# Optimization experiments

Hardware: AMD Instinct MI355X
Metric: run time of the kernel (lower is better)

## Reference

```python
import jax, jax.numpy as jnp
import numpy as np

LN_EPS = 1e-12


def setup_inputs() -> dict:
    key = jax.random.key(0)
    ks = jax.random.split(key, 10)
    B, S, W, D, H = 16, 512, 5, 200, 768
    std = 0.02
    return {
        "layer_output": jax.random.normal(ks[0], (B, S, H), dtype=jnp.float32),
        "word_embeddings": jax.random.normal(ks[1], (B, S, W, D), dtype=jnp.float32),
        "word_mask": jax.random.randint(ks[2], (B, S, W), 0, 2, dtype=jnp.int64),
        "W1": jax.random.normal(ks[3], (D, H), dtype=jnp.float32) * std,
        "b1": jnp.zeros((H,), dtype=jnp.float32),
        "W2": jax.random.normal(ks[4], (H, H), dtype=jnp.float32) * std,
        "b2": jnp.zeros((H,), dtype=jnp.float32),
        "attn_W": jax.random.normal(ks[5], (H, H), dtype=jnp.float32) * std,
        "ln_gamma": jnp.ones((H,), dtype=jnp.float32),
        "ln_beta": jnp.zeros((H,), dtype=jnp.float32),
    }


def reference(layer_output, word_embeddings, word_mask, W1, b1, W2, b2, attn_W, ln_gamma, ln_beta):
    # word_transform: Linear -> Tanh -> Linear (dropout = identity in eval)
    we = jnp.tanh(jnp.einsum("bswd,dh->bswh", word_embeddings, W1) + b1)
    we = jnp.einsum("bswh,hk->bswk", we, W2) + b2  # [B,S,W,H]

    # bilinear word attention: (x @ attn_W) . word_outputs -> score over W
    q = jnp.einsum("bsh,hk->bsk", layer_output, attn_W)  # [B,S,H]
    alpha = jnp.einsum("bsk,bswk->bsw", q, we)            # [B,S,W]
    alpha = alpha + (1.0 - word_mask.astype(alpha.dtype)) * -10000.0
    alpha = jax.nn.softmax(alpha, axis=-1)

    # weighted sum over words + residual
    agg = jnp.einsum("bsw,bswh->bsh", alpha, we)
    h = layer_output + agg

    # LayerNorm (fuse_layer; dropout = identity in eval)
    mu = jnp.mean(h, axis=-1, keepdims=True)
    var = jnp.mean(jnp.square(h - mu), axis=-1, keepdims=True)
    return (h - mu) * jax.lax.rsqrt(var + LN_EPS) * ln_gamma + ln_beta
```

## Files before the change

### kernel.cpp

```cpp
#include <hip/hip_runtime.h>
#include <hip/hip_bf16.h>
#include <math.h>


typedef __attribute__((ext_vector_type(8))) short bf16x8;
typedef __attribute__((ext_vector_type(4))) float f32x4;

__device__ __forceinline__ unsigned short f2bf_bits(float f) {
    __hip_bfloat16 h = __float2bfloat16(f);
    return *reinterpret_cast<unsigned short*>(&h);
}
__device__ __forceinline__ float bf_bits2f(unsigned short u) {
    union { unsigned int i; float f; } v; v.i = ((unsigned int)u) << 16; return v.f;
}
__device__ __forceinline__ float tanh_fast(float x) {
    float xc = fminf(fmaxf(x, -9.f), 9.f);
    float t  = __expf(2.f * xc);
    return (t - 1.f) * __builtin_amdgcn_rcpf(t + 1.f);
}

__device__ __forceinline__ void async_cp16(const void* g, void* lds) {
#if __has_builtin(__builtin_amdgcn_global_load_lds)
    auto gp = (const __attribute__((address_space(1))) unsigned int*)g;
    auto lp = (__attribute__((address_space(3))) unsigned int*)lds;
    __builtin_amdgcn_global_load_lds(gp, lp, 16, 0, 0);
#else
    *(uint4*)lds = *(const uint4*)g;
#endif
}

template<bool HAS_BIAS, bool TANH_ACT, bool RESID, bool OUT_BF16, int N, int K>
__global__ __launch_bounds__(256) void mfma_gemm(
    const __hip_bfloat16* __restrict__ A,
    const __hip_bfloat16* __restrict__ Bt,
    const float* __restrict__ bias,
    const float* __restrict__ resid,
    void* __restrict__ outp)
{
    __shared__ __align__(16) unsigned short As[128 * 32];
    __shared__ __align__(16) unsigned short Bs[128 * 32];
    const int tid  = threadIdx.x;
    const int lane = tid & 63;
    const int wave = tid >> 6;
    const int wm   = wave & 1;
    const int wn   = wave >> 1;
    const int m0   = blockIdx.y * 128;
    const int n0   = blockIdx.x * 128;

    const int srow  = lane >> 2;
    const int skoff = (lane & 3) * 8;
    const __hip_bfloat16* gA = A  + (size_t)(m0 + wave * 32 + srow) * K + skoff;
    const __hip_bfloat16* gB = Bt + (size_t)(n0 + wave * 32 + srow) * K + skoff;
    unsigned short* lA = &As[wave * 1024 + lane * 8];
    unsigned short* lB = &Bs[wave * 1024 + lane * 8];

    const int row16 = lane & 15;
    const int kq    = lane >> 4;

    f32x4 acc[4][4];
#pragma unroll
    for (int i = 0; i < 4; i++)
#pragma unroll
        for (int j = 0; j < 4; j++) acc[i][j] = (f32x4){0.f, 0.f, 0.f, 0.f};

    for (int k0 = 0; k0 < K; k0 += 32) {
        async_cp16(gA,          lA);
        async_cp16(gA + 16 * K, lA + 512);
        async_cp16(gB,          lB);
        async_cp16(gB + 16 * K, lB + 512);
        gA += 32; gB += 32;
        __syncthreads();

        bf16x8 af[4], bg[4];
#pragma unroll
        for (int mi = 0; mi < 4; mi++)
            af[mi] = *(const bf16x8*)&As[(wm * 64 + mi * 16 + row16) * 32 + kq * 8];
#pragma unroll
        for (int ni = 0; ni < 4; ni++)
            bg[ni] = *(const bf16x8*)&Bs[(wn * 64 + ni * 16 + row16) * 32 + kq * 8];
#pragma unroll
        for (int mi = 0; mi < 4; mi++)
#pragma unroll
            for (int ni = 0; ni < 4; ni++)
                acc[mi][ni] = __builtin_amdgcn_mfma_f32_16x16x32_bf16(
                    af[mi], bg[ni], acc[mi][ni], 0, 0, 0);
        __syncthreads();
    }

#pragma unroll
    for (int ni = 0; ni < 4; ni++) {
        const int gcol = n0 + wn * 64 + ni * 16 + row16;
        float bcol = 0.f;
        if (HAS_BIAS) bcol = bias[gcol];
#pragma unroll
        for (int mi = 0; mi < 4; mi++) {
#pragma unroll
            for (int r = 0; r < 4; r++) {
                const int grow = m0 + wm * 64 + mi * 16 + kq * 4 + r;
                float v = acc[mi][ni][r];
                if (HAS_BIAS) v += bcol;
                if (TANH_ACT) v = tanh_fast(v);
                if (RESID)    v += resid[(size_t)grow * N + gcol];
                if (OUT_BF16) ((__hip_bfloat16*)outp)[(size_t)grow * N + gcol] = __float2bfloat16(v);
                else          ((float*)outp)[(size_t)grow * N + gcol] = v;
            }
        }
    }
}

__global__ __launch_bounds__(256) void cvt_all(
    const float* __restrict__ x,  __hip_bfloat16* __restrict__ xb,
    const float* __restrict__ w2, __hip_bfloat16* __restrict__ w2b,
    const float* __restrict__ aw, __hip_bfloat16* __restrict__ awb)
{
    const int NX = 8192 * 768 / 4;
    const int NW = 768 * 768 / 4;
    long long i = (long long)blockIdx.x * 256 + threadIdx.x;
    const float* src; __hip_bfloat16* dst;
    if (i < NX)           { src = x;  dst = xb;  }
    else if (i < NX + NW) { src = w2; dst = w2b; i -= NX; }
    else                  { src = aw; dst = awb; i -= NX + NW; if (i >= NW) return; }
    float4 v = ((const float4*)src)[i];
    ((ushort4*)dst)[i] = make_ushort4(f2bf_bits(v.x), f2bf_bits(v.y), f2bf_bits(v.z), f2bf_bits(v.w));
}

__global__ __launch_bounds__(256) void cvt_padE(const float* __restrict__ E,
                                                __hip_bfloat16* __restrict__ Eb)
{
    const int row = blockIdx.x, k = threadIdx.x;
    if (k < 224) {
        float v = (k < 200) ? E[(size_t)row * 200 + k] : 0.f;
        Eb[(size_t)row * 224 + k] = __float2bfloat16(v);
    }
}

__global__ __launch_bounds__(256) void transpose_cvt(const float* __restrict__ in,
                                                     __hip_bfloat16* __restrict__ out,
                                                     int R, int C, int Rpad)
{
    __shared__ float tile[32][33];
    const int c0 = blockIdx.x * 32, r0 = blockIdx.y * 32;
    const int x = threadIdx.x, y = threadIdx.y;
#pragma unroll
    for (int i = 0; i < 32; i += 8) {
        int r = r0 + y + i;
        tile[y + i][x] = (r < R) ? in[(size_t)r * C + c0 + x] : 0.f;
    }
    __syncthreads();
#pragma unroll
    for (int i = 0; i < 32; i += 8)
        out[(size_t)(c0 + y + i) * Rpad + r0 + x] = __float2bfloat16(tile[x][y + i]);
}

__global__ __launch_bounds__(256) void attn_kernel(
    const __hip_bfloat16* __restrict__ T,
    const __hip_bfloat16* P,
    const int* __restrict__ mask,
    __hip_bfloat16* S)
{
    const int lane = threadIdx.x & 63;
    const int wave = threadIdx.x >> 6;
    const int r    = blockIdx.x * 4 + wave;
    const int base = lane * 12;

    float pv[12];
    {
        const ushort4* pp = (const ushort4*)((const unsigned short*)P + (size_t)r * 768 + base);
        ushort4 u0 = pp[0], u1 = pp[1], u2 = pp[2];
        unsigned short us[12] = {u0.x,u0.y,u0.z,u0.w, u1.x,u1.y,u1.z,u1.w, u2.x,u2.y,u2.z,u2.w};
#pragma unroll
        for (int j = 0; j < 12; j++) pv[j] = bf_bits2f(us[j]);
    }
    float tv[5][12], part[5];
#pragma unroll
    for (int w = 0; w < 5; w++) {
        const ushort4* tp = (const ushort4*)((const unsigned short*)T + ((size_t)r * 5 + w) * 768 + base);
        ushort4 u0 = tp[0], u1 = tp[1], u2 = tp[2];
        unsigned short us[12] = {u0.x,u0.y,u0.z,u0.w, u1.x,u1.y,u1.z,u1.w, u2.x,u2.y,u2.z,u2.w};
        float s = 0.f;
#pragma unroll
        for (int j = 0; j < 12; j++) { tv[w][j] = bf_bits2f(us[j]); s += tv[w][j] * pv[j]; }
        part[w] = s;
    }
#pragma unroll
    for (int off = 32; off > 0; off >>= 1)
#pragma unroll
        for (int w = 0; w < 5; w++)
            part[w] += __shfl_xor(part[w], off, 64);

    float logit[5], mx = -1e30f;
#pragma unroll
    for (int w = 0; w < 5; w++) {
        float m = (float)mask[(size_t)r * 5 + w];
        logit[w] = part[w] - 10000.0f * (1.0f - m);
        mx = fmaxf(mx, logit[w]);
    }
    float se = 0.f;
#pragma unroll
    for (int w = 0; w < 5; w++) { logit[w] = expf(logit[w] - mx); se += logit[w]; }
    const float inv = 1.0f / se;

    unsigned short os[12];
#pragma unroll
    for (int j = 0; j < 12; j++) {
        float s = 0.f;
#pragma unroll
        for (int w = 0; w < 5; w++) s += logit[w] * tv[w][j];
        os[j] = f2bf_bits(s * inv);
    }
    ushort4* sp = (ushort4*)((unsigned short*)S + (size_t)r * 768 + base);
    sp[0] = make_ushort4(os[0], os[1], os[2],  os[3]);
    sp[1] = make_ushort4(os[4], os[5], os[6],  os[7]);
    sp[2] = make_ushort4(os[8], os[9], os[10], os[11]);
}

__global__ __launch_bounds__(256) void ln_kernel(
    const float* __restrict__ Hbuf, const float* __restrict__ gamma,
    const float* __restrict__ beta, float* __restrict__ out)
{
    const int r = blockIdx.x, t = threadIdx.x;
    __shared__ float red[256];
    float v[3];
    float s = 0.f;
#pragma unroll
    for (int c = 0; c < 3; c++) { v[c] = Hbuf[(size_t)r * 768 + t + 256 * c]; s += v[c]; }
    red[t] = s; __syncthreads();
    for (int off = 128; off > 0; off >>= 1) { if (t < off) red[t] += red[t + off]; __syncthreads(); }
    const float mu = red[0] * (1.f / 768.f);
    __syncthreads();
    float vs = 0.f;
#pragma unroll
    for (int c = 0; c < 3; c++) { float d = v[c] - mu; vs += d * d; }
    red[t] = vs; __syncthreads();
    for (int off = 128; off > 0; off >>= 1) { if (t < off) red[t] += red[t + off]; __syncthreads(); }
    const float var = red[0] * (1.f / 768.f);
    const float rs = rsqrtf(var + 1e-12f);
#pragma unroll
    for (int c = 0; c < 3; c++) {
        int h = t + 256 * c;
        out[(size_t)r * 768 + h] = (v[c] - mu) * rs * gamma[h] + beta[h];
    }
}

extern "C" void kernel_launch(void* const* d_in, const int* in_sizes, int n_in,
                              void* d_out, int out_size, void* d_ws, size_t ws_size,
                              hipStream_t stream)
{
    const float* x      = (const float*)d_in[0];
    const float* E      = (const float*)d_in[1];
    const int*   mask   = (const int*)d_in[2];
    const float* W1     = (const float*)d_in[3];
    const float* b1     = (const float*)d_in[4];
    const float* W2     = (const float*)d_in[5];
    const float* b2     = (const float*)d_in[6];
    const float* attn_W = (const float*)d_in[7];
    const float* gamma  = (const float*)d_in[8];
    const float* beta   = (const float*)d_in[9];
    float* out = (float*)d_out;

    const int BS = 8192, H = 768, M1 = 40960, KP = 224;

    char* p = (char*)d_ws;
    auto alloc = [&](size_t bytes) { char* q = p; p += (bytes + 255) & ~(size_t)255; return q; };
    __hip_bfloat16* xb    = (__hip_bfloat16*)alloc((size_t)BS * H * 2);
    __hip_bfloat16* W2b   = (__hip_bfloat16*)alloc((size_t)H * H * 2);
    __hip_bfloat16* W2Tb  = (__hip_bfloat16*)alloc((size_t)H * H * 2);
    __hip_bfloat16* attnb = (__hip_bfloat16*)alloc((size_t)H * H * 2);
    __hip_bfloat16* Ctb   = (__hip_bfloat16*)alloc((size_t)H * H * 2);
    __hip_bfloat16* W1Tb  = (__hip_bfloat16*)alloc((size_t)H * KP * 2);
    __hip_bfloat16* Tb    = (__hip_bfloat16*)alloc((size_t)M1 * H * 2);
    __hip_bfloat16* Eb    = (__hip_bfloat16*)alloc((size_t)M1 * KP * 2);
    float* Hb = (float*)Tb;
    __hip_bfloat16* Pb = Eb;
    __hip_bfloat16* Sb = Pb;

    cvt_all<<<6144 + 576 + 576, 256, 0, stream>>>(x, xb, W2, W2b, attn_W, attnb);
    cvt_padE<<<M1, 256, 0, stream>>>(E, Eb);
    transpose_cvt<<<dim3(24, 7),  dim3(32, 8), 0, stream>>>(W1, W1Tb, 200, H, KP);
    transpose_cvt<<<dim3(24, 24), dim3(32, 8), 0, stream>>>(W2, W2Tb, H, H, H);

    mfma_gemm<false, false, false, true, 768, 768><<<dim3(6, 6), 256, 0, stream>>>(
        W2b, attnb, nullptr, nullptr, Ctb);
    mfma_gemm<true, true, false, true, 768, 224><<<dim3(6, 320), 256, 0, stream>>>(
        Eb, W1Tb, b1, nullptr, Tb);
    mfma_gemm<false, false, false, true, 768, 768><<<dim3(6, 64), 256, 0, stream>>>(
        xb, Ctb, nullptr, nullptr, Pb);
    attn_kernel<<<BS / 4, 256, 0, stream>>>(Tb, Pb, mask, Sb);
    mfma_gemm<true, false, true, false, 768, 768><<<dim3(6, 64), 256, 0, stream>>>(
        Sb, W2Tb, b2, x, Hb);
    ln_kernel<<<BS, 256, 0, stream>>>(Hb, gamma, beta, out);
}
```

Before: 264.5 us.

## Stage GEMM epilogue through LDS, remap blocks per XCD, vectorize LN and padding

The GEMM epilogue now writes results into shared memory and then stores coalesced 16-byte rows to global memory, with the residual loaded as float4. Blocks are launched on a 1D grid and remapped so consecutive tiles land on the same XCD for better L2 reuse. cvt_padE and ln_kernel are rewritten to process one row per wave with vectorized loads and wave shuffles instead of LDS tree reductions. The cost is extra LDS traffic and barriers in the epilogue, and a larger 32KB shared allocation that may reduce occupancy.

Measured after the change: 242.1 us. 1.09x faster.

```diff
diff --git a/kernel.cpp b/kernel.cpp
--- a/kernel.cpp
+++ b/kernel.cpp
@@ -29,7 +29,7 @@
 #endif
 }
 
-template<bool HAS_BIAS, bool TANH_ACT, bool RESID, bool OUT_BF16, int N, int K>
+template<bool HAS_BIAS, bool TANH_ACT, bool RESID, bool OUT_BF16, int N, int K, int GX>
 __global__ __launch_bounds__(256) void mfma_gemm(
     const __hip_bfloat16* __restrict__ A,
     const __hip_bfloat16* __restrict__ Bt,
@@ -37,22 +37,35 @@
     const float* __restrict__ resid,
     void* __restrict__ outp)
 {
-    __shared__ __align__(16) unsigned short As[128 * 32];
-    __shared__ __align__(16) unsigned short Bs[128 * 32];
+    __shared__ __align__(16) unsigned char smem[32768];
+    unsigned short* As = (unsigned short*)smem;
+    unsigned short* Bs = (unsigned short*)(smem + 8192);
+
+    int bx, by;
+    {
+        const int total = gridDim.x;
+        const int per_xcd = total >> 3;
+        if ((total & 7) == 0 && (per_xcd % GX) == 0) {
+            int xcd = blockIdx.x & 7, idx = blockIdx.x >> 3;
+            int lin = xcd * per_xcd + idx;
+            by = lin / GX; bx = lin % GX;
+        } else { by = blockIdx.x / GX; bx = blockIdx.x % GX; }
+    }
+    const int m0 = by * 128;
+    const int n0 = bx * 128;
+
     const int tid  = threadIdx.x;
     const int lane = tid & 63;
     const int wave = tid >> 6;
     const int wm   = wave & 1;
     const int wn   = wave >> 1;
-    const int m0   = blockIdx.y * 128;
-    const int n0   = blockIdx.x * 128;
 
     const int srow  = lane >> 2;
     const int skoff = (lane & 3) * 8;
     const __hip_bfloat16* gA = A  + (size_t)(m0 + wave * 32 + srow) * K + skoff;
     const __hip_bfloat16* gB = Bt + (size_t)(n0 + wave * 32 + srow) * K + skoff;
-    unsigned short* lA = &As[wave * 1024 + lane * 8];
-    unsigned short* lB = &Bs[wave * 1024 + lane * 8];
+    unsigned short* lA = As + wave * 1024 + lane * 8;
+    unsigned short* lB = Bs + wave * 1024 + lane * 8;
 
     const int row16 = lane & 15;
     const int kq    = lane >> 4;
@@ -87,23 +100,68 @@
         __syncthreads();
     }
 
-#pragma unroll
-    for (int ni = 0; ni < 4; ni++) {
-        const int gcol = n0 + wn * 64 + ni * 16 + row16;
-        float bcol = 0.f;
-        if (HAS_BIAS) bcol = bias[gcol];
-#pragma unroll
-        for (int mi = 0; mi < 4; mi++) {
-#pragma unroll
-            for (int r = 0; r < 4; r++) {
-                const int grow = m0 + wm * 64 + mi * 16 + kq * 4 + r;
-                float v = acc[mi][ni][r];
-                if (HAS_BIAS) v += bcol;
-                if (TANH_ACT) v = tanh_fast(v);
-                if (RESID)    v += resid[(size_t)grow * N + gcol];
-                if (OUT_BF16) ((__hip_bfloat16*)outp)[(size_t)grow * N + gcol] = __float2bfloat16(v);
-                else          ((float*)outp)[(size_t)grow * N + gcol] = v;
+    if (OUT_BF16) {
+        unsigned short* rep = (unsigned short*)smem;
+#pragma unroll
+        for (int ni = 0; ni < 4; ni++) {
+            const int c = wn * 64 + ni * 16 + row16;
+            float bcol = HAS_BIAS ? bias[n0 + c] : 0.f;
+#pragma unroll
+            for (int mi = 0; mi < 4; mi++)
+#pragma unroll
+                for (int r = 0; r < 4; r++) {
+                    const int rr = wm * 64 + mi * 16 + kq * 4 + r;
+                    float v = acc[mi][ni][r];
+                    if (HAS_BIAS) v += bcol;
+                    if (TANH_ACT) v = tanh_fast(v);
+                    rep[rr * 128 + c] = f2bf_bits(v);
+                }
+        }
+        __syncthreads();
+#pragma unroll
+        for (int p = 0; p < 8; p++) {
+            const int lin = p * 256 + tid;
+            const int row = lin >> 4;
+            const int c8  = lin & 15;
+            uint4 d = *(const uint4*)&rep[row * 128 + c8 * 8];
+            *(uint4*)((__hip_bfloat16*)outp + (size_t)(m0 + row) * N + n0 + c8 * 8) = d;
+        }
+    } else {
+        float* rep = (float*)smem;
+#pragma unroll
+        for (int h = 0; h < 2; h++) {
+            if (wm == h) {
+#pragma unroll
+                for (int ni = 0; ni < 4; ni++) {
+                    const int c = wn * 64 + ni * 16 + row16;
+                    float bcol = HAS_BIAS ? bias[n0 + c] : 0.f;
+#pragma unroll
+                    for (int mi = 0; mi < 4; mi++)
+#pragma unroll
+                        for (int r = 0; r < 4; r++) {
+                            const int rr = mi * 16 + kq * 4 + r;
+                            float v = acc[mi][ni][r];
+                            if (HAS_BIAS) v += bcol;
+                            if (TANH_ACT) v = tanh_fast(v);
+                            rep[rr * 128 + c] = v;
+                        }
+                }
             }
+            __syncthreads();
+#pragma unroll
+            for (int p = 0; p < 8; p++) {
+                const int lin = p * 256 + tid;
+                const int row = lin >> 5;
+                const int c4  = lin & 31;
+                float4 v = *(const float4*)&rep[row * 128 + c4 * 4];
+                const int grow = m0 + h * 64 + row;
+                if (RESID) {
+                    float4 rv = *(const float4*)&resid[(size_t)grow * N + n0 + c4 * 4];
+                    v.x += rv.x; v.y += rv.y; v.z += rv.z; v.w += rv.w;
+                }
+                *(float4*)((float*)outp + (size_t)grow * N + n0 + c4 * 4) = v;
+            }
+            __syncthreads();
         }
     }
 }
@@ -127,10 +185,15 @@
 __global__ __launch_bounds__(256) void cvt_padE(const float* __restrict__ E,
                                                 __hip_bfloat16* __restrict__ Eb)
 {
-    const int row = blockIdx.x, k = threadIdx.x;
+    const int lane = threadIdx.x & 63;
+    const int wave = threadIdx.x >> 6;
+    const long long row = (long long)blockIdx.x * 4 + wave;
+    const int k = lane * 4;
     if (k < 224) {
-        float v = (k < 200) ? E[(size_t)row * 200 + k] : 0.f;
-        Eb[(size_t)row * 224 + k] = __float2bfloat16(v);
+        float4 v = make_float4(0.f, 0.f, 0.f, 0.f);
+        if (k < 200) v = *(const float4*)&E[row * 200 + k];
+        *(ushort4*)&Eb[row * 224 + k] =
+            make_ushort4(f2bf_bits(v.x), f2bf_bits(v.y), f2bf_bits(v.z), f2bf_bits(v.w));
     }
 }
 
@@ -218,28 +281,43 @@
     const float* __restrict__ Hbuf, const float* __restrict__ gamma,
     const float* __restrict__ beta, float* __restrict__ out)
 {
-    const int r = blockIdx.x, t = threadIdx.x;
-    __shared__ float red[256];
-    float v[3];
+    const int lane = threadIdx.x & 63;
+    const int wave = threadIdx.x >> 6;
+    const int r    = blockIdx.x * 4 + wave;
+    const float* hr = Hbuf + (size_t)r * 768 + lane * 12;
+
+    float v[12];
+    {
+        float4 a = *(const float4*)(hr);
+        float4 b = *(const float4*)(hr + 4);
+        float4 c = *(const float4*)(hr + 8);
+        v[0]=a.x; v[1]=a.y; v[2]=a.z; v[3]=a.w;
+        v[4]=b.x; v[5]=b.y; v[6]=b.z; v[7]=b.w;
+        v[8]=c.x; v[9]=c.y; v[10]=c.z; v[11]=c.w;
+    }
     float s = 0.f;
 #pragma unroll
-    for (int c = 0; c < 3; c++) { v[c] = Hbuf[(size_t)r * 768 + t + 256 * c]; s += v[c]; }
-    red[t] = s; __syncthreads();
-    for (int off = 128; off > 0; off >>= 1) { if (t < off) red[t] += red[t + off]; __syncthreads(); }
-    const float mu = red[0] * (1.f / 768.f);
-    __syncthreads();
+    for (int j = 0; j < 12; j++) s += v[j];
+#pragma unroll
+    for (int off = 32; off > 0; off >>= 1) s += __shfl_xor(s, off, 64);
+    const float mu = s * (1.f / 768.f);
     float vs = 0.f;
 #pragma unroll
-    for (int c = 0; c < 3; c++) { float d = v[c] - mu; vs += d * d; }
-    red[t] = vs; __syncthreads();
-    for (int off = 128; off > 0; off >>= 1) { if (t < off) red[t] += red[t + off]; __syncthreads(); }
-    const float var = red[0] * (1.f / 768.f);
-    const float rs = rsqrtf(var + 1e-12f);
-#pragma unroll
-    for (int c = 0; c < 3; c++) {
-        int h = t + 256 * c;
-        out[(size_t)r * 768 + h] = (v[c] - mu) * rs * gamma[h] + beta[h];
-    }
+    for (int j = 0; j < 12; j++) { float d = v[j] - mu; vs += d * d; }
+#pragma unroll
+    for (int off = 32; off > 0; off >>= 1) vs += __shfl_xor(vs, off, 64);
+    const float rs = rsqrtf(vs * (1.f / 768.f) + 1e-12f);
+
+    float o[12];
+#pragma unroll
+    for (int j = 0; j < 12; j++) {
+        int h = lane * 12 + j;
+        o[j] = (v[j] - mu) * rs * gamma[h] + beta[h];
+    }
+    float* orow = out + (size_t)r * 768 + lane * 12;
+    *(float4*)(orow)     = make_float4(o[0], o[1], o[2],  o[3]);
+    *(float4*)(orow + 4) = make_float4(o[4], o[5], o[6],  o[7]);
+    *(float4*)(orow + 8) = make_float4(o[8], o[9], o[10], o[11]);
 }
 
 extern "C" void kernel_launch(void* const* d_in, const int* in_sizes, int n_in,
@@ -275,18 +353,18 @@
     __hip_bfloat16* Sb = Pb;
 
     cvt_all<<<6144 + 576 + 576, 256, 0, stream>>>(x, xb, W2, W2b, attn_W, attnb);
-    cvt_padE<<<M1, 256, 0, stream>>>(E, Eb);
+    cvt_padE<<<M1 / 4, 256, 0, stream>>>(E, Eb);
     transpose_cvt<<<dim3(24, 7),  dim3(32, 8), 0, stream>>>(W1, W1Tb, 200, H, KP);
     transpose_cvt<<<dim3(24, 24), dim3(32, 8), 0, stream>>>(W2, W2Tb, H, H, H);
 
-    mfma_gemm<false, false, false, true, 768, 768><<<dim3(6, 6), 256, 0, stream>>>(
+    mfma_gemm<false, false, false, true, 768, 768, 6><<<36, 256, 0, stream>>>(
         W2b, attnb, nullptr, nullptr, Ctb);
-    mfma_gemm<true, true, false, true, 768, 224><<<dim3(6, 320), 256, 0, stream>>>(
+    mfma_gemm<true, true, false, true, 768, 224, 6><<<1920, 256, 0, stream>>>(
         Eb, W1Tb, b1, nullptr, Tb);
-    mfma_gemm<false, false, false, true, 768, 768><<<dim3(6, 64), 256, 0, stream>>>(
+    mfma_gemm<false, false, false, true, 768, 768, 6><<<384, 256, 0, stream>>>(
         xb, Ctb, nullptr, nullptr, Pb);
     attn_kernel<<<BS / 4, 256, 0, stream>>>(Tb, Pb, mask, Sb);
-    mfma_gemm<true, false, true, false, 768, 768><<<dim3(6, 64), 256, 0, stream>>>(
+    mfma_gemm<true, false, true, false, 768, 768, 6><<<384, 256, 0, stream>>>(
         Sb, W2Tb, b2, x, Hb);
-    ln_kernel<<<BS, 256, 0, stream>>>(Hb, gamma, beta, out);
-}
+    ln_kernel<<<BS / 4, 256, 0, stream>>>(Hb, gamma, beta, out);
+}
```
